# Performance work log

Measured on AMD Instinct MI355X. Metric: run time of the kernel, lower is better.

The kernel has to match this reference:

```python
import jax, jax.numpy as jnp
import numpy as np

NUM, B, C, H, W = 2, 8, 512, 32, 32


def setup_inputs() -> dict:
    key = jax.random.key(0)
    ks = jax.random.split(key, 6)
    s = 0.02  # weight init scale
    return {
        "feat_sources": jax.random.normal(ks[0], (NUM, B, C, H, W), jnp.float32),
        "feat_targets": jax.random.normal(ks[1], (NUM, B, C, H, W), jnp.float32),
        # 1x1 conv == per-pixel channel matmul: weight [num, C_out, C_in], bias [num, C]
        "Wq": jax.random.normal(ks[2], (NUM, C, C), jnp.float32) * s,
        "bq": jnp.zeros((NUM, C), jnp.float32),
        "Wk": jax.random.normal(ks[3], (NUM, C, C), jnp.float32) * s,
        "bk": jnp.zeros((NUM, C), jnp.float32),
        "Wv": jax.random.normal(ks[4], (NUM, C, C), jnp.float32) * s,
        "bv": jnp.zeros((NUM, C), jnp.float32),
    }


def reference(feat_sources, feat_targets, Wq, bq, Wk, bk, Wv, bv):
    num, Bt, Ct, Ht, Wt = feat_targets.shape
    HW = Ht * Wt
    tgt = feat_targets.reshape(num, Bt, Ct, HW)  # queries/values come from targets
    src = feat_sources.reshape(num, Bt, Ct, HW)  # keys come from sources

    # 1x1 conv projections (batched over the `num` heads of convs)
    Q = jnp.einsum('ioc,ibcn->ibno', Wq, tgt) + bq[:, None, None, :]   # (num, B, HW, C)
    K = jnp.einsum('joc,jbcn->jbon', Wk, src) + bk[:, None, :, None]   # (num, B, C, HW)
    V = jnp.einsum('ioc,ibcn->ibon', Wv, tgt) + bv[:, None, :, None]   # (num, B, C, HW)

    # energy[i, j] = bmm(pro_query_i, pro_key_j) over all target/source pairs
    energy = jnp.einsum('ibnc,jbcm->ijbnm', Q, K)                      # (num, num, B, HW, HW)

    # alpha: softmax over sources j of the scalar mean energy per (i, j)
    means = energy.mean(axis=(2, 3, 4))                                # (num, num)
    alphas = jax.nn.softmax(means, axis=1)

    # per-source softmax over keys, then summed across sources (torch.stack(...).sum(0))
    attn = jax.nn.softmax(energy, axis=-1).sum(axis=1)                 # (num, B, HW, HW)

    # out[b, c, n] = sum_m V[b, c, m] * attn[b, n, m]  (bmm(value, attention^T))
    out = jnp.einsum('ibcm,ibnm->ibcn', V, attn).reshape(num, Bt, Ct, Ht, Wt)
    return out, alphas
```

## Files before the change

### kernel.cpp

```cpp
#include <hip/hip_runtime.h>

#define NUMH 2
#define BATCH 8
#define CCH 512
#define HWN 1024
#define LOG2E 1.4426950408889634f
#define LN2F 0.6931471805599453f

typedef unsigned short u16;
typedef unsigned int u32;
typedef _Float16 f16;
typedef __attribute__((ext_vector_type(8))) _Float16 f16x8;
typedef __attribute__((ext_vector_type(8))) short bf16x8;
typedef __attribute__((ext_vector_type(4))) float f32x4;

__device__ __forceinline__ u16 f2h(float x) {
    union { f16 h; u16 u; } cv;
    cv.h = (f16)x;
    return cv.u;
}
__device__ __forceinline__ u16 f2bf(float x) {
    u32 u = __float_as_uint(x);
    return (u16)((u + 0x7fffu + ((u >> 16) & 1u)) >> 16);
}

__device__ __forceinline__ float waveReduceSum(float v) {
#pragma unroll
    for (int off = 32; off > 0; off >>= 1) v += __shfl_xor(v, off);
    return v;
}

__device__ __forceinline__ void swz_decode(int& x, int& y, int& z) {
    const int gx = gridDim.x, gy = gridDim.y;
    const int nwg = gx * gy * gridDim.z;
    const int fid = blockIdx.x + gx * (blockIdx.y + gy * blockIdx.z);
    const int cpx = nwg >> 3;
    int swz = (fid & 7) * cpx + (fid >> 3);
    x = swz % gx; swz /= gx;
    y = swz % gy; z = swz / gy;
}

__global__ void zero_means_kernel(float* means) {
    if (threadIdx.x < 4) means[threadIdx.x] = 0.0f;
}

__global__ __launch_bounds__(256) void reduce_rs_kernel(const float* __restrict__ rs,
                                                        float* __restrict__ ls, int n) {
    const int idx = blockIdx.x * 256 + threadIdx.x;
    if (idx >= n) return;
    const int slice = idx >> 10, col = idx & 1023;
    const float* p = rs + ((size_t)slice * 16) * HWN + col;
    float s = 0.0f;
#pragma unroll
    for (int k = 0; k < 16; k++) s += p[k * HWN];
    ls[idx] = s;
}

__device__ __forceinline__ void stage_tile(const u16* __restrict__ src, int ld, int k0,
                                           u16* lds_arr, int w, int l) {
#pragma unroll
    for (int inst = 0; inst < 2; inst++) {
        const int p = w * 128 + inst * 64 + l;
        const int n = p >> 2;
        const int k4 = (p & 3) ^ ((n >> 1) & 3);
        const u16* g = src + n * ld + k0 + k4 * 8;
        u16* lp = lds_arr + (w * 128 + inst * 64) * 8;
        __builtin_amdgcn_global_load_lds(
            (const __attribute__((address_space(1))) u32*)g,
            (__attribute__((address_space(3))) u32*)lp, 16, 0, 0);
    }
}

template<bool BF>
__device__ __forceinline__ void mfma_block(const u16* sA, const u16* sB,
                                           int wr, int wc, int fr, int kq, f32x4 acc[4][4]) {
#define SLOT(row) (((row) * 4 + ((kq) ^ (((row) >> 1) & 3))) * 8)
    if constexpr (BF) {
        bf16x8 a[4], b[4];
#pragma unroll
        for (int mi = 0; mi < 4; mi++) a[mi] = *(const bf16x8*)(sA + SLOT(wr * 64 + mi * 16 + fr));
#pragma unroll
        for (int ni = 0; ni < 4; ni++) b[ni] = *(const bf16x8*)(sB + SLOT(wc * 64 + ni * 16 + fr));
#pragma unroll
        for (int mi = 0; mi < 4; mi++)
#pragma unroll
            for (int ni = 0; ni < 4; ni++)
                acc[mi][ni] = __builtin_amdgcn_mfma_f32_16x16x32_bf16(a[mi], b[ni], acc[mi][ni], 0, 0, 0);
    } else {
        f16x8 a[4], b[4];
#pragma unroll
        for (int mi = 0; mi < 4; mi++) a[mi] = *(const f16x8*)(sA + SLOT(wr * 64 + mi * 16 + fr));
#pragma unroll
        for (int ni = 0; ni < 4; ni++) b[ni] = *(const f16x8*)(sB + SLOT(wc * 64 + ni * 16 + fr));
#pragma unroll
        for (int mi = 0; mi < 4; mi++)
#pragma unroll
            for (int ni = 0; ni < 4; ni++)
                acc[mi][ni] = __builtin_amdgcn_mfma_f32_16x16x32_f16(a[mi], b[ni], acc[mi][ni], 0, 0, 0);
    }
#undef SLOT
}

template<bool BF>
__device__ __forceinline__ void mm_core(const u16* __restrict__ A, const u16* __restrict__ B,
                                        int K, int ldA, int ldB, u16* s, f32x4 acc[4][4]) {
    const int t = threadIdx.x, w = t >> 6, l = t & 63;
    const int wr = w >> 1, wc = w & 1, fr = l & 15, kq = l >> 4;
    u16 *sA0 = s, *sA1 = s + 4096, *sB0 = s + 8192, *sB1 = s + 12288;
    for (int k0 = 0; k0 < K; k0 += 64) {
        __syncthreads();
        stage_tile(A, ldA, k0, sA0, w, l);
        stage_tile(A, ldA, k0 + 32, sA1, w, l);
        stage_tile(B, ldB, k0, sB0, w, l);
        stage_tile(B, ldB, k0 + 32, sB1, w, l);
        __syncthreads();
        mfma_block<BF>(sA0, sB0, wr, wc, fr, kq, acc);
        mfma_block<BF>(sA1, sB1, wr, wc, fr, kq, acc);
    }
}

__device__ __forceinline__ void mm_core_db(const u16* __restrict__ A, const u16* __restrict__ B,
                                           int K, int ldA, int ldB, u16* s, f32x4 acc[4][4]) {
    const int t = threadIdx.x, w = t >> 6, l = t & 63;
    const int wr = w >> 1, wc = w & 1, fr = l & 15, kq = l >> 4;
    u16 *sA0 = s, *sB0 = s + 4096, *sA1 = s + 8192, *sB1 = s + 12288;
    stage_tile(A, ldA, 0, sA0, w, l);
    stage_tile(B, ldB, 0, sB0, w, l);
    __syncthreads();
    for (int k0 = 0; k0 < K; k0 += 64) {
        stage_tile(A, ldA, k0 + 32, sA1, w, l);
        stage_tile(B, ldB, k0 + 32, sB1, w, l);
        mfma_block<false>(sA0, sB0, wr, wc, fr, kq, acc);
        __syncthreads();
        if (k0 + 64 < K) {
            stage_tile(A, ldA, k0 + 64, sA0, w, l);
            stage_tile(B, ldB, k0 + 64, sB0, w, l);
        }
        mfma_block<false>(sA1, sB1, wr, wc, fr, kq, acc);
        __syncthreads();
    }
}

#define ACC_INIT(acc)                                         \
    f32x4 acc[4][4];                                          \
    _Pragma("unroll") for (int mi_ = 0; mi_ < 4; mi_++)       \
    _Pragma("unroll") for (int ni_ = 0; ni_ < 4; ni_++)       \
        acc[mi_][ni_] = (f32x4){0.f, 0.f, 0.f, 0.f};

#define SMEM_BYTES 32768

template<bool BF, bool BCOL, bool BROW>
__device__ __forceinline__ void epi_h16(char* smem, const f32x4 acc[4][4],
                                        const float* biasCol, float bcScale,
                                        const float* biasRow,
                                        u16* O, int ldO) {
    const int t = threadIdx.x, w = t >> 6, l = t & 63;
    const int wr = w >> 1, wc = w & 1, fr = l & 15, fq = l >> 4;
    u16* sb16 = (u16*)smem;
    u32* sb32 = (u32*)smem;
#pragma unroll
    for (int half = 0; half < 2; half++) {
        __syncthreads();
        if (wr == half) {
#pragma unroll
            for (int ni = 0; ni < 4; ni++) {
                const int col = wc * 64 + ni * 16 + fr;
                const float bc = BCOL ? biasCol[col] * bcScale : 0.0f;
#pragma unroll
                for (int mi = 0; mi < 4; mi++)
#pragma unroll
                    for (int r = 0; r < 4; r++) {
                        const int lrow = mi * 16 + fq * 4 + r;
                        const float v = acc[mi][ni][r] + bc +
                                        (BROW ? biasRow[half * 64 + lrow] : 0.0f);
                        sb16[lrow * 132 + col] = BF ? f2bf(v) : f2h(v);
                    }
            }
        }
        __syncthreads();
#pragma unroll
        for (int it = 0; it < 4; it++) {
            const int idx = it * 256 + t;
            const int rr = idx >> 4, ch = idx & 15;
            const uint4 v4 = *(const uint4*)&sb32[rr * 66 + ch * 4];
            *(uint4*)&O[(size_t)(half * 64 + rr) * ldO + ch * 8] = v4;
        }
    }
}

template<bool SCALE>
__device__ __forceinline__ void epi_f32(char* smem, const f32x4 acc[4][4],
                                        const float* ls, float* O, int ldO) {
    const int t = threadIdx.x, w = t >> 6, l = t & 63;
    const int wr = w >> 1, wc = w & 1, fr = l & 15, fq = l >> 4;
    float* sf = (float*)smem;
#pragma unroll
    for (int q = 0; q < 4; q++) {
        __syncthreads();
        if (wr == (q >> 1)) {
            const int mi0 = (q & 1) * 2;
#pragma unroll
            for (int ni = 0; ni < 4; ni++) {
                const int col = wc * 64 + ni * 16 + fr;
                const float inv = SCALE ? 1.0f / ls[col] : 1.0f;
#pragma unroll
                for (int mm = 0; mm < 2; mm++)
#pragma unroll
                    for (int r = 0; r < 4; r++) {
                        const int lrow = mm * 16 + fq * 4 + r;
                        sf[lrow * 132 + col] = acc[mi0 + mm][ni][r] * inv;
                    }
            }
        }
        __syncthreads();
#pragma unroll
        for (int it = 0; it < 4; it++) {
            const int idx = it * 256 + t;
            const int rr = idx >> 5, ch = idx & 31;
            const float4 v4 = *(const float4*)&sf[rr * 132 + ch * 4];
            *(float4*)&O[(size_t)(q * 32 + rr) * ldO + ch * 4] = v4;
        }
    }
}

__global__ __launch_bounds__(256) void tconv_kernel(
    const float* __restrict__ tgt, const float* __restrict__ src,
    u16* __restrict__ Tt, u16* __restrict__ St) {
    __shared__ float s[64][65];
    const int z = blockIdx.z;
    const int ib = z & 15;
    const float* X = (z >> 4 ? src : tgt) + (size_t)ib * CCH * HWN;
    u16* O = (z >> 4 ? St : Tt) + (size_t)ib * HWN * CCH;
    const int n0 = blockIdx.x * 64, c0 = blockIdx.y * 64;
    const int t = threadIdx.x;
    {
        const int cc = t >> 4, nch = (t & 15) * 4;
#pragma unroll
        for (int r = 0; r < 4; r++) {
            const float4 v = *(const float4*)&X[(size_t)(c0 + cc + r * 16) * HWN + n0 + nch];
            s[cc + r * 16][nch + 0] = v.x;
            s[cc + r * 16][nch + 1] = v.y;
            s[cc + r * 16][nch + 2] = v.z;
            s[cc + r * 16][nch + 3] = v.w;
        }
    }
    __syncthreads();
    const int nl = t >> 2;
    const int cb = (t & 3) * 16;
    __attribute__((aligned(16))) u16 hbuf[16];
#pragma unroll
    for (int cc = 0; cc < 16; cc++) hbuf[cc] = f2h(s[cb + cc][nl]);
    const size_t orow = (size_t)(n0 + nl) * CCH + c0 + cb;
    *(uint4*)&O[orow + 0] = *(const uint4*)&hbuf[0];
    *(uint4*)&O[orow + 8] = *(const uint4*)&hbuf[8];
}

__global__ __launch_bounds__(256) void convw_kernel(
    const float* __restrict__ Wq, const float* __restrict__ Wk, const float* __restrict__ Wv,
    u16* __restrict__ Wqh, u16* __restrict__ Wkh, u16* __restrict__ Wvh) {
    const int idx = (blockIdx.x * 256 + threadIdx.x) * 4;
    {
        const float4 v = *(const float4*)&Wq[idx];
        uint2 h = {(u32)f2h(v.x * LOG2E) | ((u32)f2h(v.y * LOG2E) << 16),
                   (u32)f2h(v.z * LOG2E) | ((u32)f2h(v.w * LOG2E) << 16)};
        *(uint2*)&Wqh[idx] = h;
    }
    {
        const float4 v = *(const float4*)&Wk[idx];
        uint2 h = {(u32)f2h(v.x) | ((u32)f2h(v.y) << 16), (u32)f2h(v.z) | ((u32)f2h(v.w) << 16)};
        *(uint2*)&Wkh[idx] = h;
    }
    {
        const float4 v = *(const float4*)&Wv[idx];
        uint2 h = {(u32)f2h(v.x) | ((u32)f2h(v.y) << 16), (u32)f2h(v.z) | ((u32)f2h(v.w) << 16)};
        *(uint2*)&Wvh[idx] = h;
    }
}

__global__ __launch_bounds__(256) void proj_qk_kernel(
    const u16* __restrict__ Tt, const u16* __restrict__ St,
    const u16* __restrict__ Wqh, const u16* __restrict__ Wkh,
    const float* __restrict__ bq, const float* __restrict__ bk,
    u16* __restrict__ Qp, u16* __restrict__ Kp) {
    __shared__ __align__(16) char smem[SMEM_BYTES];
    int bx, by, z;
    swz_decode(bx, by, z);
    const int b = z & 7, i = (z >> 3) & 1, p = z >> 4;
    const size_t ib = (size_t)(i * BATCH + b) * HWN * CCH;
    const u16* A = (p ? St : Tt) + ib;
    const u16* B = (p ? Wkh : Wqh) + (size_t)i * CCH * CCH;
    const float* bias = (p ? bk : bq) + i * CCH;
    u16* O = (p ? Kp : Qp) + ib;
    const int tile_m = by * 128, tile_n = bx * 128;

    ACC_INIT(acc)
    mm_core<false>(A + (size_t)tile_m * CCH, B + (size_t)tile_n * CCH,
                   CCH, CCH, CCH, (u16*)smem, acc);

    epi_h16<false, true, false>(smem, acc, bias + tile_n, p ? 1.0f : LOG2E, nullptr,
                                O + (size_t)tile_m * CCH + tile_n, CCH);
}

__global__ __launch_bounds__(256) void proj_v_kernel(
    const u16* __restrict__ Wvh, const u16* __restrict__ Tt,
    const float* __restrict__ bvv, u16* __restrict__ Vb) {
    __shared__ __align__(16) char smem[SMEM_BYTES];
    int bx, by, z;
    swz_decode(bx, by, z);
    const int b = z & 7, i = z >> 3;
    const size_t ib = (size_t)(i * BATCH + b) * HWN * CCH;
    const u16* A = Wvh + (size_t)i * CCH * CCH;
    const u16* B = Tt + ib;
    const int tile_m = by * 128, tile_n = bx * 128;

    ACC_INIT(acc)
    mm_core<false>(A + (size_t)tile_m * CCH, B + (size_t)tile_n * CCH,
                   CCH, CCH, CCH, (u16*)smem, acc);

    u16* Ov = Vb + (size_t)(i * BATCH + b) * CCH * HWN;
    epi_h16<true, false, true>(smem, acc, nullptr, 1.0f, bvv + i * CCH + tile_m,
                               Ov + (size_t)tile_m * HWN + tile_n, HWN);
}

__global__ __launch_bounds__(256) void gemmE_kernel(
    const u16* __restrict__ Qp, const u16* __restrict__ Kp,
    u16* __restrict__ P, float* __restrict__ rs, float* __restrict__ means,
    int b0, int Bc) {
    __shared__ __align__(16) char smem[33792];
    __shared__ float redsum[4];
    int bx, by, z;
    swz_decode(bx, by, z);
    const int j = z & 1, ib2 = z >> 1;
    const int i = ib2 / Bc, bb = ib2 % Bc, b = b0 + bb;
    const size_t offA = (size_t)(i * BATCH + b) * HWN * CCH;
    const size_t offB = (size_t)(j * BATCH + b) * HWN * CCH;
    const int tile_m = by * 128, tile_n = bx * 128;
    u16* Po = P + (size_t)(ib2 * 2 + j) * HWN * HWN + (size_t)tile_m * HWN + tile_n;

    ACC_INIT(acc)
    mm_core_db(Qp + offA + (size_t)tile_m * CCH, Kp + offB + (size_t)tile_n * CCH,
               CCH, CCH, CCH, (u16*)smem, acc);

    const int t = threadIdx.x, w = t >> 6, l = t & 63;
    const int wr = w >> 1, wc = w & 1, fr = l & 15, fq = l >> 4;
    u16* sb16 = (u16*)smem;
    u32* sb32 = (u32*)smem;
    float* rsp = rs + ((size_t)(ib2 * 2 + j) * 16 + (bx * 2 + wc)) * HWN;
    float tsum = 0.0f;
    float rowacc[4][4];
#pragma unroll
    for (int mi = 0; mi < 4; mi++)
#pragma unroll
        for (int r = 0; r < 4; r++) rowacc[mi][r] = 0.0f;
#pragma unroll
    for (int ni = 0; ni < 4; ni++) {
        const int col = wc * 64 + ni * 16 + fr;
#pragma unroll
        for (int mi = 0; mi < 4; mi++)
#pragma unroll
            for (int r = 0; r < 4; r++) {
                const int row = wr * 64 + mi * 16 + fq * 4 + r;
                const float raw = acc[mi][ni][r];
                tsum += raw;
                const float ex = exp2f(raw);
                rowacc[mi][r] += ex;
                sb16[row * 132 + col] = f2bf(ex);
            }
    }
    __syncthreads();
#pragma unroll
    for (int it = 0; it < 8; it++) {
        const int idx = it * 256 + t;
        const int rr = idx >> 4, ch = idx & 15;
        const uint4 v4 = *(const uint4*)&sb32[rr * 66 + ch * 4];
        *(uint4*)&Po[(size_t)rr * HWN + ch * 8] = v4;
    }
    tsum = waveReduceSum(tsum);
    if (l == 0) redsum[w] = tsum;
#pragma unroll
    for (int mi = 0; mi < 4; mi++)
#pragma unroll
        for (int r = 0; r < 4; r++) {
            float v = rowacc[mi][r];
            v += __shfl_xor(v, 1); v += __shfl_xor(v, 2);
            v += __shfl_xor(v, 4); v += __shfl_xor(v, 8);
            if (fr == 0) rsp[tile_m + wr * 64 + mi * 16 + fq * 4 + r] = v;
        }
    __syncthreads();
    if (t == 0) atomicAdd(&means[i * 2 + j], redsum[0] + redsum[1] + redsum[2] + redsum[3]);
}

__global__ __launch_bounds__(256) void gemmOut_kernel(
    const u16* __restrict__ Vb, const u16* __restrict__ P, const float* __restrict__ ls,
    float* __restrict__ outp, int b0, int Bc) {
    __shared__ __align__(16) char smem[SMEM_BYTES];
    int bx, by, ib2;
    swz_decode(bx, by, ib2);
    const int i = ib2 / Bc, bb = ib2 % Bc, b = b0 + bb;
    const u16* A = Vb + (size_t)(i * BATCH + b) * CCH * HWN;
    const u16* P0 = P + (size_t)(ib2 * 2 + 0) * HWN * HWN;
    const u16* P1 = P + (size_t)(ib2 * 2 + 1) * HWN * HWN;
    const float* ls0 = ls + (size_t)(ib2 * 2 + 0) * HWN;
    const float* ls1 = ls + (size_t)(ib2 * 2 + 1) * HWN;
    float* O = outp + (size_t)(i * BATCH + b) * CCH * HWN;
    const int tile_m = by * 128, tile_n = bx * 128;
    const int t = threadIdx.x, w = t >> 6, l = t & 63;
    const int wc = w & 1, fr = l & 15;

    ACC_INIT(acc)
    mm_core<true>(A + (size_t)tile_m * HWN, P0 + (size_t)tile_n * HWN,
                  HWN, HWN, HWN, (u16*)smem, acc);
#pragma unroll
    for (int ni = 0; ni < 4; ni++) {
        const int col = tile_n + wc * 64 + ni * 16 + fr;
        const float sc = ls1[col] / ls0[col];
#pragma unroll
        for (int mi = 0; mi < 4; mi++) acc[mi][ni] *= sc;
    }
    mm_core<true>(A + (size_t)tile_m * HWN, P1 + (size_t)tile_n * HWN,
                  HWN, HWN, HWN, (u16*)smem, acc);

    epi_f32<true>(smem, acc, ls1 + tile_n, O + (size_t)tile_m * HWN + tile_n, HWN);
}

__global__ void alphas_kernel(const float* __restrict__ means, float* __restrict__ outp) {
    if (threadIdx.x != 0) return;
    const float cnt = (float)BATCH * (float)HWN * (float)HWN;
    float m[4];
#pragma unroll
    for (int k = 0; k < 4; k++) m[k] = means[k] / cnt * LN2F;
#pragma unroll
    for (int i = 0; i < 2; i++) {
        const float a = m[i * 2 + 0], bsc = m[i * 2 + 1];
        const float mx = fmaxf(a, bsc);
        const float ea = __expf(a - mx), eb = __expf(bsc - mx);
        const float inv = 1.0f / (ea + eb);
        outp[i * 2 + 0] = ea * inv;
        outp[i * 2 + 1] = eb * inv;
    }
}

extern "C" void kernel_launch(void* const* d_in, const int* in_sizes, int n_in,
                              void* d_out, int out_size, void* d_ws, size_t ws_size,
                              hipStream_t stream) {
    const float* fsrc = (const float*)d_in[0];
    const float* ftgt = (const float*)d_in[1];
    const float* Wq = (const float*)d_in[2];
    const float* bq = (const float*)d_in[3];
    const float* Wk = (const float*)d_in[4];
    const float* bk = (const float*)d_in[5];
    const float* Wv = (const float*)d_in[6];
    const float* bv = (const float*)d_in[7];
    float* outp = (float*)d_out;

    const size_t SZ_ACT = (size_t)NUMH * BATCH * HWN * CCH * 2;
    const size_t SZ_W = (size_t)NUMH * CCH * CCH * 2;
    char* w = (char*)d_ws;
    u16* Qp = (u16*)w; w += SZ_ACT;
    u16* Kp = (u16*)w; w += SZ_ACT;
    u16* Vb = (u16*)w; w += SZ_ACT;
    u16* Wqh = (u16*)w; w += SZ_W;
    u16* Wkh = (u16*)w; w += SZ_W;
    u16* Wvh = (u16*)w; w += SZ_W;
    float* means = (float*)w; w += 64;
    float* rs = (float*)w; w += (size_t)NUMH * BATCH * 2 * 16 * HWN * 4;
    float* ls = (float*)w; w += (size_t)NUMH * BATCH * 2 * HWN * 4;
    char* region = w;
    u16* Tt = (u16*)region;
    u16* St = (u16*)(region + SZ_ACT);

    const size_t base_used = (size_t)(region - (char*)d_ws);
    int Bc = 8;
    while (Bc > 1) {
        size_t need = (size_t)NUMH * Bc * 2 * HWN * HWN * 2;
        size_t tneed = need > 2 * SZ_ACT ? need : 2 * SZ_ACT;
        if (base_used + tneed <= ws_size) break;
        Bc >>= 1;
    }
    u16* P = (u16*)region;

    zero_means_kernel<<<1, 64, 0, stream>>>(means);
    convw_kernel<<<512, 256, 0, stream>>>(Wq, Wk, Wv, Wqh, Wkh, Wvh);
    tconv_kernel<<<dim3(16, 8, 32), 256, 0, stream>>>(ftgt, fsrc, Tt, St);
    proj_qk_kernel<<<dim3(4, 8, 32), 256, 0, stream>>>(Tt, St, Wqh, Wkh, bq, bk, Qp, Kp);
    proj_v_kernel<<<dim3(8, 4, 16), 256, 0, stream>>>(Wvh, Tt, bv, Vb);

    const int nch = BATCH / Bc;
    for (int ch = 0; ch < nch; ch++) {
        const int b0 = ch * Bc;
        const int nls = NUMH * Bc * 2 * HWN;
        gemmE_kernel<<<dim3(8, 8, NUMH * Bc * 2), 256, 0, stream>>>(Qp, Kp, P, rs, means, b0, Bc);
        reduce_rs_kernel<<<(nls + 255) / 256, 256, 0, stream>>>(rs, ls, nls);
        gemmOut_kernel<<<dim3(8, 4, NUMH * Bc), 256, 0, stream>>>(Vb, P, ls, outp, b0, Bc);
    }
    alphas_kernel<<<1, 1, 0, stream>>>(means, outp + (out_size - 4));
}
```

Measured before the change: 202.2 us.

## Triple-buffer energy GEMM main loop with vmcnt-based waits instead of full barriers

Replaces the double-buffered K loop of the energy GEMM with a three-stage shared-memory ring that is fully unrolled over the 16 K-steps. Each step waits with explicit s_waitcnt vmcnt counts rather than draining all outstanding loads, which lets global loads for later stages stay in flight while MFMAs run. Shared memory per block grows from 33 KB to 48 KB, which may lower occupancy. The code relies on the exact number of global load instructions per stage_tile for the hard-coded vmcnt values to be correct.

```diff
diff --git a/kernel.cpp b/kernel.cpp
--- a/kernel.cpp
+++ b/kernel.cpp
@@ -119,25 +119,33 @@
     }
 }
 
-__device__ __forceinline__ void mm_core_db(const u16* __restrict__ A, const u16* __restrict__ B,
-                                           int K, int ldA, int ldB, u16* s, f32x4 acc[4][4]) {
+#define VMCNT(n) asm volatile("s_waitcnt vmcnt(" #n ")" ::: "memory")
+#define LGKM0()  asm volatile("s_waitcnt lgkmcnt(0)" ::: "memory")
+__device__ __forceinline__ void mm_core_cnt(const u16* __restrict__ A, const u16* __restrict__ B,
+                                            int ldA, int ldB, u16* s, f32x4 acc[4][4]) {
     const int t = threadIdx.x, w = t >> 6, l = t & 63;
     const int wr = w >> 1, wc = w & 1, fr = l & 15, kq = l >> 4;
-    u16 *sA0 = s, *sB0 = s + 4096, *sA1 = s + 8192, *sB1 = s + 12288;
-    stage_tile(A, ldA, 0, sA0, w, l);
-    stage_tile(B, ldB, 0, sB0, w, l);
-    __syncthreads();
-    for (int k0 = 0; k0 < K; k0 += 64) {
-        stage_tile(A, ldA, k0 + 32, sA1, w, l);
-        stage_tile(B, ldB, k0 + 32, sB1, w, l);
-        mfma_block<false>(sA0, sB0, wr, wc, fr, kq, acc);
-        __syncthreads();
-        if (k0 + 64 < K) {
-            stage_tile(A, ldA, k0 + 64, sA0, w, l);
-            stage_tile(B, ldB, k0 + 64, sB0, w, l);
-        }
-        mfma_block<false>(sA1, sB1, wr, wc, fr, kq, acc);
-        __syncthreads();
+    stage_tile(A, ldA, 0, s, w, l);
+    stage_tile(B, ldB, 0, s + 4096, w, l);
+    stage_tile(A, ldA, 32, s + 8192, w, l);
+    stage_tile(B, ldB, 32, s + 12288, w, l);
+    stage_tile(A, ldA, 64, s + 16384, w, l);
+    stage_tile(B, ldB, 64, s + 20480, w, l);
+#pragma unroll
+    for (int st = 0; st < 16; st++) {
+        if (st < 14) { VMCNT(8); } else if (st == 14) { VMCNT(4); } else { VMCNT(0); }
+        __builtin_amdgcn_s_barrier();
+        __builtin_amdgcn_sched_barrier(0);
+        u16* base = s + (st % 3) * 8192;
+        mfma_block<false>(base, base + 4096, wr, wc, fr, kq, acc);
+        LGKM0();
+        __builtin_amdgcn_sched_barrier(0);
+        __builtin_amdgcn_s_barrier();
+        __builtin_amdgcn_sched_barrier(0);
+        if (st + 3 < 16) {
+            stage_tile(A, ldA, (st + 3) * 32, base, w, l);
+            stage_tile(B, ldB, (st + 3) * 32, base + 4096, w, l);
+        }
     }
 }
 
@@ -326,7 +334,7 @@
     const u16* __restrict__ Qp, const u16* __restrict__ Kp,
     u16* __restrict__ P, float* __restrict__ rs, float* __restrict__ means,
     int b0, int Bc) {
-    __shared__ __align__(16) char smem[33792];
+    __shared__ __align__(16) char smem[49152];
     __shared__ float redsum[4];
     int bx, by, z;
     swz_decode(bx, by, z);
@@ -338,14 +346,15 @@
     u16* Po = P + (size_t)(ib2 * 2 + j) * HWN * HWN + (size_t)tile_m * HWN + tile_n;
 
     ACC_INIT(acc)
-    mm_core_db(Qp + offA + (size_t)tile_m * CCH, Kp + offB + (size_t)tile_n * CCH,
-               CCH, CCH, CCH, (u16*)smem, acc);
+    mm_core_cnt(Qp + offA + (size_t)tile_m * CCH, Kp + offB + (size_t)tile_n * CCH,
+                CCH, CCH, (u16*)smem, acc);
 
     const int t = threadIdx.x, w = t >> 6, l = t & 63;
     const int wr = w >> 1, wc = w & 1, fr = l & 15, fq = l >> 4;
     u16* sb16 = (u16*)smem;
     u32* sb32 = (u32*)smem;
     float* rsp = rs + ((size_t)(ib2 * 2 + j) * 16 + (bx * 2 + wc)) * HWN;
+    __syncthreads();
     float tsum = 0.0f;
     float rowacc[4][4];
 #pragma unroll
```

Result: no change. 205.0 us (+1.4%).
